# Kernel tuning notes

Hardware: AMD Instinct MI355X
Metric: run time of the kernel (lower is better)

The kernel has to match this reference:

```python
import jax, jax.numpy as jnp
import numpy as np
from jax import lax

B, T, C, H, HOR = 64, 2048, 64, 256, 96
BETA, THR = 0.9, 1.0


def setup_inputs() -> dict:
    key = jax.random.key(0)
    ks = jax.random.split(key, 10)
    s = lambda *sh: 1.0 / np.sqrt(sh[-1])
    return {
        "x": jax.random.normal(ks[0], (B, T, C), jnp.float32),
        "snn_w": jax.random.uniform(ks[1], (H, C), jnp.float32, -s(C), s(C)),
        "snn_b": jax.random.uniform(ks[2], (H,), jnp.float32, -s(C), s(C)),
        "gru_wih": jax.random.uniform(ks[3], (3 * H, C + H), jnp.float32, -s(H), s(H)),
        "gru_whh": jax.random.uniform(ks[4], (3 * H, H), jnp.float32, -s(H), s(H)),
        "gru_bih": jax.random.uniform(ks[5], (3 * H,), jnp.float32, -s(H), s(H)),
        "gru_bhh": jax.random.uniform(ks[6], (3 * H,), jnp.float32, -s(H), s(H)),
        "head_w": jax.random.uniform(ks[7], (HOR, H), jnp.float32, -s(H), s(H)),
        "head_b": jax.random.uniform(ks[8], (HOR,), jnp.float32, -s(H), s(H)),
    }


@jax.custom_vjp
def spike(x):
    return (x > 0).astype(x.dtype)

def _spike_fwd(x):
    return spike(x), x

def _spike_bwd(x, g):
    # snntorch ATan surrogate, alpha=2: grad = 1 / (1 + (pi*x)^2)
    return (g / (1.0 + (jnp.pi * x) ** 2),)

spike.defvjp(_spike_fwd, _spike_bwd)


def reference(x, snn_w, snn_b, gru_wih, gru_whh, gru_bih, gru_bhh, head_w, head_b):
    # Batched SNN input current across all timesteps: [B,T,H]
    cur = jnp.einsum("btc,hc->bth", x, snn_w) + snn_b

    def lif_step(mem, i_t):
        # reset computed from previous mem, detached (snntorch mem_reset)
        reset = lax.stop_gradient((mem > THR).astype(mem.dtype))
        mem_new = BETA * mem + i_t - reset * THR
        spk = spike(mem_new - THR)
        return mem_new, spk

    mem0 = jnp.zeros((B, H), x.dtype)
    _, spks = lax.scan(lif_step, mem0, cur.transpose(1, 0, 2))  # [T,B,H]

    h_comb = jnp.concatenate([x, spks.transpose(1, 0, 2)], axis=-1)  # [B,T,C+H]

    # GRU: precompute input gates for all timesteps
    gx = jnp.einsum("btc,gc->btg", h_comb, gru_wih) + gru_bih  # [B,T,3H]

    def gru_step(h, gx_t):
        gh = h @ gru_whh.T + gru_bhh
        xr, xz, xn = jnp.split(gx_t, 3, axis=-1)
        hr, hz, hn = jnp.split(gh, 3, axis=-1)
        r = jax.nn.sigmoid(xr + hr)
        z = jax.nn.sigmoid(xz + hz)
        n = jnp.tanh(xn + r * hn)
        h_new = (1.0 - z) * n + z * h
        return h_new, None

    h0 = jnp.zeros((B, H), x.dtype)
    hT, _ = lax.scan(gru_step, h0, gx.transpose(1, 0, 2))

    return hT @ head_w.T + head_b  # [B, HOR]
```

## Files before the change

### kernel.cpp

```cpp
#include <hip/hip_runtime.h>
#include <cstdint>
#include <cstddef>

#define B_   64
#define T_   2048
#define C_   64
#define H_   256
#define G3_  768
#define HOR_ 96

typedef _Float16 h2 __attribute__((ext_vector_type(2)));
typedef _Float16 h8 __attribute__((ext_vector_type(8)));
typedef _Float16 f16x8 __attribute__((ext_vector_type(8)));
typedef float f32x4 __attribute__((ext_vector_type(4)));

__global__ void k_zero(int* __restrict__ flags) { flags[threadIdx.x] = 0; }

#define K1_TT 128
__global__ __launch_bounds__(256) void k_cur(const float* __restrict__ x,
                                             const float* __restrict__ w,
                                             const float* __restrict__ bias,
                                             float* __restrict__ cur) {
  __shared__ float xs[K1_TT * C_];
  const int b = blockIdx.x;
  const int t0 = blockIdx.y * K1_TT;
  const int tid = threadIdx.x;

  const float4* xsrc = (const float4*)(x + ((size_t)b * T_ + t0) * C_);
  float4* xdst = (float4*)xs;
#pragma unroll
  for (int i = 0; i < (K1_TT * C_ / 4) / 256; i++)
    xdst[tid + i * 256] = xsrc[tid + i * 256];

  float wr[C_];
  const float4* wp = (const float4*)(w + (size_t)tid * C_);
#pragma unroll
  for (int q = 0; q < C_ / 4; q++) {
    float4 v = wp[q];
    wr[4 * q + 0] = v.x; wr[4 * q + 1] = v.y;
    wr[4 * q + 2] = v.z; wr[4 * q + 3] = v.w;
  }
  const float bb = bias[tid];
  __syncthreads();

  for (int t = 0; t < K1_TT; t++) {
    const float4* xrow = (const float4*)(xs + t * C_);
    float a0 = 0.f, a1 = 0.f;
#pragma unroll
    for (int q = 0; q < C_ / 4; q += 2) {
      float4 v0 = xrow[q];
      float4 v1 = xrow[q + 1];
      a0 += wr[4 * q + 0] * v0.x + wr[4 * q + 1] * v0.y +
            wr[4 * q + 2] * v0.z + wr[4 * q + 3] * v0.w;
      a1 += wr[4 * q + 4] * v1.x + wr[4 * q + 5] * v1.y +
            wr[4 * q + 6] * v1.z + wr[4 * q + 7] * v1.w;
    }
    cur[((size_t)b * T_ + t0 + t) * H_ + tid] = a0 + a1 + bb;
  }
}

__global__ __launch_bounds__(64) void k_lif(const float* __restrict__ cur,
                                            unsigned char* __restrict__ spk) {
  const int b = blockIdx.x >> 2;
  const int h = ((blockIdx.x & 3) << 6) + threadIdx.x;
  const float* cp = cur + (size_t)b * T_ * H_ + h;
  unsigned char* sp = spk + (size_t)b * T_ * H_ + h;
  float mem = 0.f;
#pragma unroll 8
  for (int t = 0; t < T_; t++) {
    float c = cp[(size_t)t * H_];
    float reset = (mem > 1.0f) ? 1.0f : 0.0f;
    mem = 0.9f * mem + c - reset;
    sp[(size_t)t * H_] = (mem > 1.0f) ? (unsigned char)1 : (unsigned char)0;
  }
}

#define GM 128
#define GN 128
#define AKP 40
#define CTP 136
#define DQ_ (0.0625f / (127.0f * 127.0f))
__global__ __launch_bounds__(512) void k_fused(
    const float* __restrict__ x, const unsigned char* __restrict__ spk,
    const float* __restrict__ wih, const float* __restrict__ bih,
    _Float16* __restrict__ gx, const float* __restrict__ whh,
    const float* __restrict__ bhh, const float* __restrict__ head_w,
    const float* __restrict__ head_b, float* __restrict__ out,
    int* __restrict__ flags) {
  alignas(16) __shared__ _Float16 Ah[GM * AKP];
  alignas(16) __shared__ _Float16 Bh[GN * AKP];
  alignas(16) __shared__ _Float16 Ct[GM * CTP];
  alignas(16) __shared__ int hq[2][64];
  __shared__ float hbuf32[H_];

  const int tid = threadIdx.x;
  const int lane = tid & 63;

  if (blockIdx.x >= 64) {
    const int pidx = blockIdx.x - 64;
    const int bb = pidx / 3;
    const int pp = pidx - bb * 3;
    const int wave = tid >> 6;
    const int ln = lane & 15;
    const int qd = lane >> 4;
    const int wm = (wave & 1) * 64;
    const int wn = ((wave >> 1) & 1) * 64;

    for (int mt = 0; mt < 16; mt++) {
      const int m0 = bb * 2048 + mt * 128;
      for (int nh = 0; nh < 2; nh++) {
        const int n0 = pp * 256 + nh * 128;
        f32x4 acc[4][4] = {};
        for (int kc = 0; kc < 10; kc++) {
          const int k0 = kc * 32;
          if (tid < 256) {
            if (k0 < 64) {
#pragma unroll
              for (int i = 0; i < 4; i++) {
                int idx = tid + i * 256;
                int r = idx >> 3;
                int c4 = (idx & 7) * 4;
                float4 v = *(const float4*)(x + (size_t)(m0 + r) * C_ + k0 + c4);
                h2 lo, hi;
                lo.x = (_Float16)v.x; lo.y = (_Float16)v.y;
                hi.x = (_Float16)v.z; hi.y = (_Float16)v.w;
                h2* d = (h2*)&Ah[r * AKP + c4];
                d[0] = lo; d[1] = hi;
              }
            } else {
#pragma unroll
              for (int i = 0; i < 4; i++) {
                int idx = tid + i * 256;
                int r = idx >> 3;
                int c4 = (idx & 7) * 4;
                uchar4 u = *(const uchar4*)(spk + (size_t)(m0 + r) * H_ + (k0 - 64) + c4);
                h2 lo, hi;
                lo.x = (_Float16)(int)u.x; lo.y = (_Float16)(int)u.y;
                hi.x = (_Float16)(int)u.z; hi.y = (_Float16)(int)u.w;
                h2* d = (h2*)&Ah[r * AKP + c4];
                d[0] = lo; d[1] = hi;
              }
            }
#pragma unroll
            for (int i = 0; i < 4; i++) {
              int idx = tid + i * 256;
              int r = idx >> 3;
              int c4 = (idx & 7) * 4;
              float4 v = *(const float4*)(wih + (size_t)(n0 + r) * 320 + k0 + c4);
              h2 lo, hi;
              lo.x = (_Float16)v.x; lo.y = (_Float16)v.y;
              hi.x = (_Float16)v.z; hi.y = (_Float16)v.w;
              h2* d = (h2*)&Bh[r * AKP + c4];
              d[0] = lo; d[1] = hi;
            }
          }
          __syncthreads();
          if (tid < 256) {
            f16x8 a[4], bbf[4];
#pragma unroll
            for (int mtl = 0; mtl < 4; mtl++)
              a[mtl] = *(const f16x8*)&Ah[(wm + mtl * 16 + ln) * AKP + qd * 8];
#pragma unroll
            for (int nt = 0; nt < 4; nt++)
              bbf[nt] = *(const f16x8*)&Bh[(wn + nt * 16 + ln) * AKP + qd * 8];
#pragma unroll
            for (int mtl = 0; mtl < 4; mtl++)
#pragma unroll
              for (int nt = 0; nt < 4; nt++)
                acc[mtl][nt] = __builtin_amdgcn_mfma_f32_16x16x32_f16(
                    a[mtl], bbf[nt], acc[mtl][nt], 0, 0, 0);
          }
          __syncthreads();
        }
        if (tid < 256) {
          float bias[4];
#pragma unroll
          for (int nt = 0; nt < 4; nt++) bias[nt] = bih[n0 + wn + nt * 16 + ln];
#pragma unroll
          for (int mtl = 0; mtl < 4; mtl++)
#pragma unroll
            for (int nt = 0; nt < 4; nt++) {
              int n = wn + nt * 16 + ln;
#pragma unroll
              for (int r = 0; r < 4; r++) {
                int m = wm + mtl * 16 + qd * 4 + r;
                Ct[m * CTP + n] = (_Float16)(acc[mtl][nt][r] + bias[nt]);
              }
            }
        }
        __syncthreads();
        if (tid < 256) {
#pragma unroll
          for (int i = 0; i < 8; i++) {
            int idx = tid + i * 256;
            int r = idx >> 4;
            int c = (idx & 15) * 8;
            *(h8*)(gx + (size_t)(m0 + r) * G3_ + n0 + c) = *(const h8*)&Ct[r * CTP + c];
          }
        }
        __syncthreads();
      }
      if (tid == 0)
        __hip_atomic_fetch_add(&flags[bb * 16 + mt], 1, __ATOMIC_RELEASE,
                               __HIP_MEMORY_SCOPE_AGENT);
    }
    return;
  }

  const int b = blockIdx.x;
  const int wave = tid >> 6;
  const int j = wave * 32 + (lane >> 1);
  const int kq = lane & 1;
  const int k0 = kq * 128;

  int wr[32], wz[32], wn[32];
  {
    const float qs = 2032.0f;
    const float4* p0 = (const float4*)(whh + (size_t)j * H_ + k0);
    const float4* p1 = (const float4*)(whh + (size_t)(H_ + j) * H_ + k0);
    const float4* p2 = (const float4*)(whh + (size_t)(2 * H_ + j) * H_ + k0);
#pragma unroll
    for (int q = 0; q < 32; q++) {
      float4 a = p0[q];
      wr[q] = ((int)rintf(a.x * qs) & 255) | (((int)rintf(a.y * qs) & 255) << 8) |
              (((int)rintf(a.z * qs) & 255) << 16) | (((int)rintf(a.w * qs) & 255) << 24);
      float4 c = p1[q];
      wz[q] = ((int)rintf(c.x * qs) & 255) | (((int)rintf(c.y * qs) & 255) << 8) |
              (((int)rintf(c.z * qs) & 255) << 16) | (((int)rintf(c.w * qs) & 255) << 24);
      float4 d = p2[q];
      wn[q] = ((int)rintf(d.x * qs) & 255) | (((int)rintf(d.y * qs) & 255) << 8) |
              (((int)rintf(d.z * qs) & 255) << 16) | (((int)rintf(d.w * qs) & 255) << 24);
    }
  }
  const float br_ = bhh[j], bz_ = bhh[H_ + j], bn_ = bhh[2 * H_ + j];

  if (tid < 128) ((int*)hq)[tid] = 0;
  float hj = 0.f;
  __syncthreads();

  const _Float16* gxb = gx + (size_t)b * T_ * G3_;
  int p = 0;
  for (int mt = 0; mt < 16; mt++) {
    if (tid == 0) {
      while (__hip_atomic_load(&flags[b * 16 + mt], __ATOMIC_ACQUIRE,
                               __HIP_MEMORY_SCOPE_AGENT) < 3)
        __builtin_amdgcn_s_sleep(8);
    }
    __syncthreads();

    const _Float16* gc = gxb + (size_t)mt * 128 * G3_;
    _Float16 pr = gc[j], pz = gc[H_ + j], pn = gc[2 * H_ + j];

    for (int tt = 0; tt < 128; tt++) {
      float xr = (float)pr, xz = (float)pz, xn = (float)pn;
      if (tt < 127) {
        const _Float16* g = gc + (size_t)(tt + 1) * G3_;
        pr = g[j]; pz = g[H_ + j]; pn = g[2 * H_ + j];
      }

      const int* hb = &hq[p][kq * 32];
      int ar = 0, az = 0, an = 0;
#pragma unroll
      for (int g4 = 0; g4 < 4; g4++) {
#pragma unroll
        for (int cc = 0; cc < 2; cc++) {
          int c = g4 * 2 + cc;
          int4 hv = *(const int4*)(hb + c * 4);
#pragma unroll
          for (int i = 0; i < 4; i++) {
            int h4 = (i == 0) ? hv.x : (i == 1) ? hv.y : (i == 2) ? hv.z : hv.w;
            int wi = c * 4 + i;
            ar = __builtin_amdgcn_sdot4(wr[wi], h4, ar, false);
            az = __builtin_amdgcn_sdot4(wz[wi], h4, az, false);
            an = __builtin_amdgcn_sdot4(wn[wi], h4, an, false);
          }
        }
        __builtin_amdgcn_sched_barrier(2 | 4 | 16 | 32 | 64);
      }
      ar += __shfl_xor(ar, 1, 64);
      az += __shfl_xor(az, 1, 64);
      an += __shfl_xor(an, 1, 64);

      float r = 1.f / (1.f + __expf(-(xr + (float)ar * DQ_ + br_)));
      float z = 1.f / (1.f + __expf(-(xz + (float)az * DQ_ + bz_)));
      float pre = xn + r * ((float)an * DQ_ + bn_);
      float e = __expf(2.f * pre);
      float n = 1.f - 2.f / (e + 1.f);
      hj = (1.f - z) * n + z * hj;

      if (kq == 0) ((char*)hq[p ^ 1])[j] = (char)(int)rintf(hj * 127.0f);
      p ^= 1;
      __syncthreads();
    }
  }

  if (kq == 0) hbuf32[j] = hj;
  __syncthreads();

  if (tid < HOR_) {
    const float4* hw = (const float4*)(head_w + (size_t)tid * H_);
    const float4* hv4 = (const float4*)hbuf32;
    float acc = head_b[tid];
#pragma unroll
    for (int q = 0; q < H_ / 4; q++) {
      float4 w4 = hw[q];
      float4 v4 = hv4[q];
      acc += w4.x * v4.x + w4.y * v4.y + w4.z * v4.z + w4.w * v4.w;
    }
    out[(size_t)b * HOR_ + tid] = acc;
  }
}

extern "C" void kernel_launch(void* const* d_in, const int* in_sizes, int n_in,
                              void* d_out, int out_size, void* d_ws, size_t ws_size,
                              hipStream_t stream) {
  const float* x      = (const float*)d_in[0];
  const float* snn_w  = (const float*)d_in[1];
  const float* snn_b  = (const float*)d_in[2];
  const float* wih    = (const float*)d_in[3];
  const float* whh    = (const float*)d_in[4];
  const float* bih    = (const float*)d_in[5];
  const float* bhh    = (const float*)d_in[6];
  const float* head_w = (const float*)d_in[7];
  const float* head_b = (const float*)d_in[8];
  float* out = (float*)d_out;

  char* ws = (char*)d_ws;
  _Float16* gx = (_Float16*)ws;
  float* cur = (float*)ws;
  unsigned char* spk = (unsigned char*)(ws + (size_t)201326592);
  int* flags = (int*)(ws + (size_t)234881024);

  k_zero<<<1, 1024, 0, stream>>>(flags);
  k_cur<<<dim3(B_, T_ / K1_TT), 256, 0, stream>>>(x, snn_w, snn_b, cur);
  k_lif<<<dim3(256), 64, 0, stream>>>(cur, spk);
  k_fused<<<dim3(256), 512, 0, stream>>>(x, spk, wih, bih, gx, whh, bhh,
                                         head_w, head_b, out, flags);
}
```

Baseline: 1.995 ms.

## Process two batch sequences per GRU recurrence block to share weight registers

Each recurrence block now advances two batch rows at once, reusing the register-resident int8 Whh weights for both dot-product chains, and the grid shrinks from 256 to 224 blocks (32 recurrence plus 192 GEMM producers). Interleaving two independent chains is meant to hide sdot4 and barrier latency and halve the per-step sync overhead per sequence. In exchange each step does twice the work on the serial critical path, and there are half as many recurrence blocks, which may lengthen the total serial time.

```diff
diff --git a/kernel.cpp b/kernel.cpp
--- a/kernel.cpp
+++ b/kernel.cpp
@@ -90,14 +90,14 @@
   alignas(16) __shared__ _Float16 Ah[GM * AKP];
   alignas(16) __shared__ _Float16 Bh[GN * AKP];
   alignas(16) __shared__ _Float16 Ct[GM * CTP];
-  alignas(16) __shared__ int hq[2][64];
-  __shared__ float hbuf32[H_];
+  alignas(16) __shared__ int hq[2][2][64];
+  __shared__ float hbuf32[2][H_];
 
   const int tid = threadIdx.x;
   const int lane = tid & 63;
 
-  if (blockIdx.x >= 64) {
-    const int pidx = blockIdx.x - 64;
+  if (blockIdx.x >= 32) {
+    const int pidx = blockIdx.x - 32;
     const int bb = pidx / 3;
     const int pp = pidx - bb * 3;
     const int wave = tid >> 6;
@@ -207,7 +207,8 @@
     return;
   }
 
-  const int b = blockIdx.x;
+  const int cb = blockIdx.x;
+  const int bA = cb * 2, bB = cb * 2 + 1;
   const int wave = tid >> 6;
   const int j = wave * 32 + (lane >> 1);
   const int kq = lane & 1;
@@ -234,80 +235,112 @@
   }
   const float br_ = bhh[j], bz_ = bhh[H_ + j], bn_ = bhh[2 * H_ + j];
 
-  if (tid < 128) ((int*)hq)[tid] = 0;
-  float hj = 0.f;
+  if (tid < 256) ((int*)hq)[tid] = 0;
+  float hjA = 0.f, hjB = 0.f;
   __syncthreads();
 
-  const _Float16* gxb = gx + (size_t)b * T_ * G3_;
+  const _Float16* gxA = gx + (size_t)bA * T_ * G3_;
+  const _Float16* gxB = gx + (size_t)bB * T_ * G3_;
   int p = 0;
   for (int mt = 0; mt < 16; mt++) {
     if (tid == 0) {
-      while (__hip_atomic_load(&flags[b * 16 + mt], __ATOMIC_ACQUIRE,
+      while (__hip_atomic_load(&flags[bA * 16 + mt], __ATOMIC_ACQUIRE,
+                               __HIP_MEMORY_SCOPE_AGENT) < 3 ||
+             __hip_atomic_load(&flags[bB * 16 + mt], __ATOMIC_ACQUIRE,
                                __HIP_MEMORY_SCOPE_AGENT) < 3)
         __builtin_amdgcn_s_sleep(8);
     }
     __syncthreads();
 
-    const _Float16* gc = gxb + (size_t)mt * 128 * G3_;
-    _Float16 pr = gc[j], pz = gc[H_ + j], pn = gc[2 * H_ + j];
+    const _Float16* gcA = gxA + (size_t)mt * 128 * G3_;
+    const _Float16* gcB = gxB + (size_t)mt * 128 * G3_;
+    _Float16 prA = gcA[j], pzA = gcA[H_ + j], pnA = gcA[2 * H_ + j];
+    _Float16 prB = gcB[j], pzB = gcB[H_ + j], pnB = gcB[2 * H_ + j];
 
     for (int tt = 0; tt < 128; tt++) {
-      float xr = (float)pr, xz = (float)pz, xn = (float)pn;
+      float xrA = (float)prA, xzA = (float)pzA, xnA = (float)pnA;
+      float xrB = (float)prB, xzB = (float)pzB, xnB = (float)pnB;
       if (tt < 127) {
-        const _Float16* g = gc + (size_t)(tt + 1) * G3_;
-        pr = g[j]; pz = g[H_ + j]; pn = g[2 * H_ + j];
-      }
-
-      const int* hb = &hq[p][kq * 32];
-      int ar = 0, az = 0, an = 0;
+        const _Float16* gA = gcA + (size_t)(tt + 1) * G3_;
+        const _Float16* gB = gcB + (size_t)(tt + 1) * G3_;
+        prA = gA[j]; pzA = gA[H_ + j]; pnA = gA[2 * H_ + j];
+        prB = gB[j]; pzB = gB[H_ + j]; pnB = gB[2 * H_ + j];
+      }
+
+      const int* hbA = &hq[0][p][kq * 32];
+      const int* hbB = &hq[1][p][kq * 32];
+      int arA = 0, azA = 0, anA = 0, arB = 0, azB = 0, anB = 0;
 #pragma unroll
       for (int g4 = 0; g4 < 4; g4++) {
 #pragma unroll
         for (int cc = 0; cc < 2; cc++) {
           int c = g4 * 2 + cc;
-          int4 hv = *(const int4*)(hb + c * 4);
+          int4 hvA = *(const int4*)(hbA + c * 4);
+          int4 hvB = *(const int4*)(hbB + c * 4);
 #pragma unroll
           for (int i = 0; i < 4; i++) {
-            int h4 = (i == 0) ? hv.x : (i == 1) ? hv.y : (i == 2) ? hv.z : hv.w;
+            int hA = (i == 0) ? hvA.x : (i == 1) ? hvA.y : (i == 2) ? hvA.z : hvA.w;
+            int hB = (i == 0) ? hvB.x : (i == 1) ? hvB.y : (i == 2) ? hvB.z : hvB.w;
             int wi = c * 4 + i;
-            ar = __builtin_amdgcn_sdot4(wr[wi], h4, ar, false);
-            az = __builtin_amdgcn_sdot4(wz[wi], h4, az, false);
-            an = __builtin_amdgcn_sdot4(wn[wi], h4, an, false);
+            arA = __builtin_amdgcn_sdot4(wr[wi], hA, arA, false);
+            arB = __builtin_amdgcn_sdot4(wr[wi], hB, arB, false);
+            azA = __builtin_amdgcn_sdot4(wz[wi], hA, azA, false);
+            azB = __builtin_amdgcn_sdot4(wz[wi], hB, azB, false);
+            anA = __builtin_amdgcn_sdot4(wn[wi], hA, anA, false);
+            anB = __builtin_amdgcn_sdot4(wn[wi], hB, anB, false);
           }
         }
         __builtin_amdgcn_sched_barrier(2 | 4 | 16 | 32 | 64);
       }
-      ar += __shfl_xor(ar, 1, 64);
-      az += __shfl_xor(az, 1, 64);
-      an += __shfl_xor(an, 1, 64);
-
-      float r = 1.f / (1.f + __expf(-(xr + (float)ar * DQ_ + br_)));
-      float z = 1.f / (1.f + __expf(-(xz + (float)az * DQ_ + bz_)));
-      float pre = xn + r * ((float)an * DQ_ + bn_);
-      float e = __expf(2.f * pre);
-      float n = 1.f - 2.f / (e + 1.f);
-      hj = (1.f - z) * n + z * hj;
-
-      if (kq == 0) ((char*)hq[p ^ 1])[j] = (char)(int)rintf(hj * 127.0f);
+      arA += __shfl_xor(arA, 1, 64); azA += __shfl_xor(azA, 1, 64);
+      anA += __shfl_xor(anA, 1, 64);
+      arB += __shfl_xor(arB, 1, 64); azB += __shfl_xor(azB, 1, 64);
+      anB += __shfl_xor(anB, 1, 64);
+
+      {
+        float r = 1.f / (1.f + __expf(-(xrA + (float)arA * DQ_ + br_)));
+        float z = 1.f / (1.f + __expf(-(xzA + (float)azA * DQ_ + bz_)));
+        float pre = xnA + r * ((float)anA * DQ_ + bn_);
+        float e = __expf(2.f * pre);
+        float n = 1.f - 2.f / (e + 1.f);
+        hjA = (1.f - z) * n + z * hjA;
+      }
+      {
+        float r = 1.f / (1.f + __expf(-(xrB + (float)arB * DQ_ + br_)));
+        float z = 1.f / (1.f + __expf(-(xzB + (float)azB * DQ_ + bz_)));
+        float pre = xnB + r * ((float)anB * DQ_ + bn_);
+        float e = __expf(2.f * pre);
+        float n = 1.f - 2.f / (e + 1.f);
+        hjB = (1.f - z) * n + z * hjB;
+      }
+
+      if (kq == 0) {
+        ((char*)hq[0][p ^ 1])[j] = (char)(int)rintf(hjA * 127.0f);
+        ((char*)hq[1][p ^ 1])[j] = (char)(int)rintf(hjB * 127.0f);
+      }
       p ^= 1;
       __syncthreads();
     }
   }
 
-  if (kq == 0) hbuf32[j] = hj;
+  if (kq == 0) { hbuf32[0][j] = hjA; hbuf32[1][j] = hjB; }
   __syncthreads();
 
-  if (tid < HOR_) {
-    const float4* hw = (const float4*)(head_w + (size_t)tid * H_);
-    const float4* hv4 = (const float4*)hbuf32;
-    float acc = head_b[tid];
-#pragma unroll
-    for (int q = 0; q < H_ / 4; q++) {
-      float4 w4 = hw[q];
-      float4 v4 = hv4[q];
-      acc += w4.x * v4.x + w4.y * v4.y + w4.z * v4.z + w4.w * v4.w;
-    }
-    out[(size_t)b * HOR_ + tid] = acc;
+  {
+    const int bsel = tid >> 8;
+    const int o = tid & 255;
+    if (o < HOR_) {
+      const float4* hw = (const float4*)(head_w + (size_t)o * H_);
+      const float4* hv4 = (const float4*)hbuf32[bsel];
+      float acc = head_b[o];
+#pragma unroll
+      for (int q = 0; q < H_ / 4; q++) {
+        float4 w4 = hw[q];
+        float4 v4 = hv4[q];
+        acc += w4.x * v4.x + w4.y * v4.y + w4.z * v4.z + w4.w * v4.w;
+      }
+      out[(size_t)(bA + bsel) * HOR_ + o] = acc;
+    }
   }
 }
 
@@ -334,6 +367,6 @@
   k_zero<<<1, 1024, 0, stream>>>(flags);
   k_cur<<<dim3(B_, T_ / K1_TT), 256, 0, stream>>>(x, snn_w, snn_b, cur);
   k_lif<<<dim3(256), 64, 0, stream>>>(cur, spk);
-  k_fused<<<dim3(256), 512, 0, stream>>>(x, spk, wih, bih, gx, whh, bhh,
+  k_fused<<<dim3(224), 512, 0, stream>>>(x, spk, wih, bih, gx, whh, bhh,
                                          head_w, head_b, out, flags);
 }
```

After: 3.271 ms. 1.64x slower.
